# Performance work log

Measured on AMD Instinct MI355X. Metric: run time of the kernel, lower is better.

The kernel has to match this reference:

```python
import jax, jax.numpy as jnp
import numpy as np

B, L, R, A, E = 256, 64, 1024, 512, 1024


def lstm_cell(x, h, c, W_ih, W_hh, b_ih, b_hh):
    # PyTorch LSTMCell gate order: i, f, g, o
    gates = x @ W_ih.T + b_ih + h @ W_hh.T + b_hh
    i, f, g, o = jnp.split(gates, 4, axis=1)
    c2 = jax.nn.sigmoid(f) * c + jax.nn.sigmoid(i) * jnp.tanh(g)
    h2 = jax.nn.sigmoid(o) * jnp.tanh(c2)
    return h2, c2


def attend(h, wh_w, wh_b, wa_w, wa_b, feats_proj, feats_value):
    # Bahdanau attention: tanh(Wh h + proj(feats)) -> scalar logit -> softmax -> weighted sum
    dot = jnp.tanh(feats_proj + (h @ wh_w.T + wh_b)[:, None, :])  # [B,L,A]
    logits = jnp.einsum('bla,a->bl', dot, wa_w[0]) + wa_b[0]      # [B,L]
    w = jax.nn.softmax(logits, axis=1)
    return jnp.einsum('bl,bld->bd', w, feats_value)


def setup_inputs() -> dict:
    key = jax.random.key(0)
    ks = iter(jax.random.split(key, 64))
    rn = lambda shape, s=1.0: jax.random.normal(next(ks), shape, dtype=jnp.float32) * s
    inp = {
        'xt': rn((B, E)),
        'fc_feats': rn((B, R)),
        'roi_feats': rn((B, L, R)),
        'p_roi_feats': rn((B, L, A)),
        'context_feats': rn((B, L, R)),
        'state_h': rn((2, B, R)),
        'state_c': rn((2, B, R)),
        # scco (visual) LSTM: input E + 2R
        'W_ih_v': rn((4 * R, E + 2 * R), 0.02), 'W_hh_v': rn((4 * R, R), 0.02),
        'b_ih_v': rn((4 * R,), 0.02), 'b_hh_v': rn((4 * R,), 0.02),
        # language LSTM: input 2R
        'W_ih_l': rn((4 * R, 2 * R), 0.02), 'W_hh_l': rn((4 * R, R), 0.02),
        'b_ih_l': rn((4 * R,), 0.02), 'b_hh_l': rn((4 * R,), 0.02),
        # SingleSP: wh, wa
        'sp_wh_w': rn((A, R), 0.02), 'sp_wh_b': rn((A,), 0.02),
        'sp_wa_w': rn((1, A), 0.02), 'sp_wa_b': rn((1,), 0.02),
        # ContextSP: wh, wv, wa
        'ctx_wh_w': rn((A, R), 0.02), 'ctx_wh_b': rn((A,), 0.02),
        'ctx_wv_w': rn((A, R), 0.02), 'ctx_wv_b': rn((A,), 0.02),
        'ctx_wa_w': rn((1, A), 0.02), 'ctx_wa_b': rn((1,), 0.02),
        # CompSP: wh, wv, wa
        'cmp_wh_w': rn((A, R), 0.02), 'cmp_wh_b': rn((A,), 0.02),
        'cmp_wv_w': rn((A, R), 0.02), 'cmp_wv_b': rn((A,), 0.02),
        'cmp_wa_w': rn((1, A), 0.02), 'cmp_wa_b': rn((1,), 0.02),
        # OutputSP: wv, wh, wa
        'out_wv_w': rn((A, R), 0.02), 'out_wv_b': rn((A,), 0.02),
        'out_wh_w': rn((A, R), 0.02), 'out_wh_b': rn((A,), 0.02),
        'out_wa_w': rn((1, A), 0.02), 'out_wa_b': rn((1,), 0.02),
    }
    return inp


def reference(xt, fc_feats, roi_feats, p_roi_feats, context_feats, state_h, state_c,
              W_ih_v, W_hh_v, b_ih_v, b_hh_v, W_ih_l, W_hh_l, b_ih_l, b_hh_l,
              sp_wh_w, sp_wh_b, sp_wa_w, sp_wa_b,
              ctx_wh_w, ctx_wh_b, ctx_wv_w, ctx_wv_b, ctx_wa_w, ctx_wa_b,
              cmp_wh_w, cmp_wh_b, cmp_wv_w, cmp_wv_b, cmp_wa_w, cmp_wa_b,
              out_wv_w, out_wv_b, out_wh_w, out_wh_b, out_wa_w, out_wa_b):
    prev_h = state_h[-1]
    env = jnp.concatenate([prev_h, fc_feats, xt], axis=1)  # [B, 2R+E]
    h_vis, c_vis = lstm_cell(env, state_h[0], state_c[0], W_ih_v, W_hh_v, b_ih_v, b_hh_v)

    # SingleSP: attend over rois using precomputed projections p_roi_feats
    single_feat = attend(h_vis, sp_wh_w, sp_wh_b, sp_wa_w, sp_wa_b, p_roi_feats, roi_feats)

    # ContextSP: attend over context_feats
    ctx_proj = context_feats @ ctx_wv_w.T + ctx_wv_b
    context_feat = attend(h_vis, ctx_wh_w, ctx_wh_b, ctx_wa_w, ctx_wa_b, ctx_proj, context_feats)

    # CompSP: attend over relation feats = context - roi
    rel = context_feat[:, None, :] - roi_feats  # [B,L,R]
    rel_proj = rel @ cmp_wv_w.T + cmp_wv_b
    comp_feat = attend(h_vis, cmp_wh_w, cmp_wh_b, cmp_wa_w, cmp_wa_b, rel_proj, rel)

    # OutputSP: attend over {single, comp, fc}
    feats3 = jnp.stack([single_feat, comp_feat, fc_feats], axis=1)  # [B,3,R]
    f3_proj = feats3 @ out_wv_w.T + out_wv_b
    output_feats = attend(h_vis, out_wh_w, out_wh_b, out_wa_w, out_wa_b, f3_proj, feats3)

    lang_in = jnp.concatenate([output_feats, h_vis], axis=1)  # [B,2R]
    h_lang, c_lang = lstm_cell(lang_in, state_h[1], state_c[1], W_ih_l, W_hh_l, b_ih_l, b_hh_l)

    output = h_lang  # dropout is identity in eval mode
    new_h = jnp.stack([h_vis, h_lang])
    new_c = jnp.stack([c_vis, c_lang])
    return output, new_h, new_c, output_feats
```

## Files before the change

kernel.cpp:

```cpp
#include <hip/hip_runtime.h>
#include <hip/hip_bf16.h>
#include <math.h>

#define B_ 256
#define L_ 64
#define R_ 1024
#define A_ 512
#define E_ 1024
#define BR (B_ * R_)

typedef __attribute__((ext_vector_type(8))) short short8;
typedef __attribute__((ext_vector_type(4))) float f32x4;

__device__ __forceinline__ unsigned int pkbf(float x, float y) {
    union { __hip_bfloat162 h; unsigned int u; } cv;
    cv.h = __float22bfloat162_rn(make_float2(x, y));
    return cv.u;
}

__device__ __forceinline__ float tanh_fast(float x) {
    return 1.f - 2.f / (1.f + __expf(2.f * x));
}
__device__ __forceinline__ float sigm_(float x) { return 1.f / (1.f + __expf(-x)); }

__device__ __forceinline__ void mm_core(const float* __restrict__ Abm, int lda,
                                        const float* __restrict__ Wbn, int ldw,
                                        int K, f32x4 acc[4][4])
{
    __shared__ unsigned int As[2][2048];
    __shared__ unsigned int Ws[2][2048];

    const int t = threadIdx.x;
    const int srow = t >> 3, sub = t & 7;
    const int half = sub & 1;
    const int csw = (sub >> 1) ^ ((srow >> 1) & 3);
    int sidx[4];
    const float* pa[4];
    const float* pw[4];
#pragma unroll
    for (int i = 0; i < 4; ++i) {
        int row = srow + 32 * i;
        sidx[i] = row * 16 + csw * 4 + half * 2;
        pa[i] = Abm + (size_t)row * lda + sub * 4;
        pw[i] = Wbn + (size_t)row * ldw + sub * 4;
    }
    const int w = t >> 6, lane = t & 63;
    const int m0 = (w >> 1) * 64, n0 = (w & 1) * 64;
    const int lrow = lane & 15, quad = lane >> 4;
    int aidx[4], widx[4];
#pragma unroll
    for (int i = 0; i < 4; ++i) {
        int ra = m0 + i * 16 + lrow;
        aidx[i] = ra * 16 + ((quad ^ ((ra >> 1) & 3)) << 2);
        int rw = n0 + i * 16 + lrow;
        widx[i] = rw * 16 + ((quad ^ ((rw >> 1) & 3)) << 2);
    }

    float4 ra4[4], rw4[4];
#define MMC_LOAD() do { _Pragma("unroll") for (int i = 0; i < 4; ++i) { \
        ra4[i] = *(const float4*)pa[i]; rw4[i] = *(const float4*)pw[i]; \
        pa[i] += 32; pw[i] += 32; } } while (0)
#define MMC_STORE(buf) do { _Pragma("unroll") for (int i = 0; i < 4; ++i) { \
        *(uint2*)(As[buf] + sidx[i]) = make_uint2(pkbf(ra4[i].x, ra4[i].y), pkbf(ra4[i].z, ra4[i].w)); \
        *(uint2*)(Ws[buf] + sidx[i]) = make_uint2(pkbf(rw4[i].x, rw4[i].y), pkbf(rw4[i].z, rw4[i].w)); } } while (0)

    const int n = K >> 5;
    MMC_LOAD();
    MMC_STORE(0);
    MMC_LOAD();
    for (int k = 0; k < n; ++k) {
        __syncthreads();
        short8 af[4], wf[4];
#pragma unroll
        for (int i = 0; i < 4; ++i) {
            af[i] = *(const short8*)(As[k & 1] + aidx[i]);
            wf[i] = *(const short8*)(Ws[k & 1] + widx[i]);
        }
        if (k + 1 < n) {
            MMC_STORE((k + 1) & 1);
            if (k + 2 < n) MMC_LOAD();
        }
#pragma unroll
        for (int mt = 0; mt < 4; ++mt)
#pragma unroll
            for (int nt = 0; nt < 4; ++nt)
                acc[mt][nt] = __builtin_amdgcn_mfma_f32_16x16x32_bf16(
                    af[mt], wf[nt], acc[mt][nt], 0, 0, 0);
    }
#undef MMC_LOAD
#undef MMC_STORE
}

__device__ __forceinline__ void mm_store(f32x4 acc[4][4], float* __restrict__ Cbm,
                                         int ldc, int bn, const float* __restrict__ bias)
{
    const int t = threadIdx.x;
    const int w = t >> 6, lane = t & 63;
    const int m0 = (w >> 1) * 64, n0 = (w & 1) * 64;
    const int lrow = lane & 15, quad = lane >> 4;
#pragma unroll
    for (int nt = 0; nt < 4; ++nt) {
        int col = bn + n0 + nt * 16 + lrow;
        float bv = bias ? bias[col] : 0.f;
#pragma unroll
        for (int mt = 0; mt < 4; ++mt) {
            int rbase = m0 + mt * 16 + quad * 4;
#pragma unroll
            for (int r = 0; r < 4; ++r)
                Cbm[(size_t)(rbase + r) * ldc + col] = acc[mt][nt][r] + bv;
        }
    }
}

__device__ __forceinline__ void attn_epilogue(
    f32x4 acc[4][4], int bm, int bn, int M, int L,
    const float* __restrict__ base, const float* __restrict__ base2,
    const float* __restrict__ wbias, const float* __restrict__ wa,
    float sign, float* __restrict__ lpart)
{
    __shared__ float lsum[2][128];
    const int t = threadIdx.x;
    const int w = t >> 6, lane = t & 63;
    const int m0 = (w >> 1) * 64, n0 = (w & 1) * 64;
    const int lrow = lane & 15, quad = lane >> 4;
    float wav[4], wbv[4];
    int colv[4];
#pragma unroll
    for (int nt = 0; nt < 4; ++nt) {
        colv[nt] = bn + n0 + nt * 16 + lrow;
        wav[nt] = wa[colv[nt]];
        wbv[nt] = wbias ? wbias[colv[nt]] : 0.f;
    }
#pragma unroll
    for (int mt = 0; mt < 4; ++mt) {
#pragma unroll
        for (int r = 0; r < 4; ++r) {
            int rl = m0 + mt * 16 + quad * 4 + r;
            int row = bm + rl;
            int b = row / L;
            const float* bp = base + (size_t)b * A_;
            const float* bp2 = base2 ? base2 + (size_t)b * A_ : nullptr;
            float s = 0.f;
#pragma unroll
            for (int nt = 0; nt < 4; ++nt) {
                float v = bp[colv[nt]] + wbv[nt] + sign * acc[mt][nt][r];
                if (bp2) v += bp2[colv[nt]];
                s += tanh_fast(v) * wav[nt];
            }
            s += __shfl_xor(s, 1);
            s += __shfl_xor(s, 2);
            s += __shfl_xor(s, 4);
            s += __shfl_xor(s, 8);
            if (lrow == 0) lsum[w & 1][rl] = s;
        }
    }
    __syncthreads();
    if (t < 128)
        lpart[(size_t)(bn >> 7) * M + bm + t] = lsum[0][t] + lsum[1][t];
}

struct Seg8 { const float* A[8]; const float* W[8]; int lda[8]; int ldw[8]; };

__global__ __launch_bounds__(256) void mm_seg(Seg8 s, float* __restrict__ Cbase,
                                              int ldc, int kchunk, int zstride)
{
    int z = blockIdx.z;
    int bm = blockIdx.y * 128, bn = blockIdx.x * 128;
    f32x4 acc[4][4];
#pragma unroll
    for (int i = 0; i < 4; ++i)
#pragma unroll
        for (int j = 0; j < 4; ++j) acc[i][j] = (f32x4)0.f;
    mm_core(s.A[z] + (size_t)bm * s.lda[z], s.lda[z],
            s.W[z] + (size_t)bn * s.ldw[z], s.ldw[z], kchunk, acc);
    mm_store(acc, Cbase + (size_t)z * zstride + (size_t)bm * ldc, ldc, bn, nullptr);
}

struct Jobs4 { const float* A[4]; const float* W[4]; const float* bias[4]; float* C[4]; };
__global__ __launch_bounds__(256) void mm_jobs(Jobs4 p, int K)
{
    int z = blockIdx.z;
    int bm = blockIdx.y * 128, bn = blockIdx.x * 128;
    f32x4 acc[4][4];
#pragma unroll
    for (int i = 0; i < 4; ++i)
#pragma unroll
        for (int j = 0; j < 4; ++j) acc[i][j] = (f32x4)0.f;
    mm_core(p.A[z] + (size_t)bm * 1024, 1024, p.W[z] + (size_t)bn * 1024, 1024, K, acc);
    mm_store(acc, p.C[z] + (size_t)bm * 512, 512, bn, p.bias[z]);
}

__global__ __launch_bounds__(256) void mm_fused_attn(
    const float* __restrict__ A, int lda, const float* __restrict__ W, int ldw, int K,
    const float* __restrict__ base, const float* __restrict__ base2,
    const float* __restrict__ wbias, const float* __restrict__ wa,
    float sign, int M, int L, float* __restrict__ lpart)
{
    int bm = blockIdx.y * 128, bn = blockIdx.x * 128;
    f32x4 acc[4][4];
#pragma unroll
    for (int i = 0; i < 4; ++i)
#pragma unroll
        for (int j = 0; j < 4; ++j) acc[i][j] = (f32x4)0.f;
    mm_core(A + (size_t)bm * lda, lda, W + (size_t)bn * ldw, ldw, K, acc);
    attn_epilogue(acc, bm, bn, M, L, base, base2, wbias, wa, sign, lpart);
}

__global__ __launch_bounds__(256) void attn_logits_sp(
    const float* __restrict__ base, const float* __restrict__ proj,
    const float* __restrict__ wa, float* __restrict__ logits)
{
    int idx = blockIdx.x * 4 + (threadIdx.x >> 6);
    int lane = threadIdx.x & 63;
    int b = idx >> 6;
    const f32x4* p = (const f32x4*)(proj + (size_t)idx * A_);
    const f32x4* bs = (const f32x4*)(base + (size_t)b * A_);
    const f32x4* wv = (const f32x4*)wa;
    float acc = 0.f;
#pragma unroll
    for (int i = 0; i < 2; ++i) {
        int a = i * 64 + lane;
        f32x4 pv = p[a], bv = bs[a], w4 = wv[a];
#pragma unroll
        for (int j = 0; j < 4; ++j) acc += tanh_fast(bv[j] + pv[j]) * w4[j];
    }
#pragma unroll
    for (int off = 32; off > 0; off >>= 1) acc += __shfl_xor(acc, off);
    if (lane == 0) logits[idx] = acc;
}

__global__ __launch_bounds__(256) void softmax_part(
    const float* __restrict__ lpart, int np, int M, int L, float* __restrict__ attw)
{
    int grp = blockIdx.x * 4 + (threadIdx.x >> 6);
    int lane = threadIdx.x & 63;
    int row = grp * L + lane;
    float v = -INFINITY;
    if (lane < L) {
        float s = 0.f;
        for (int p = 0; p < np; ++p) s += lpart[(size_t)p * M + row];
        v = s;
    }
    float m = v;
#pragma unroll
    for (int off = 32; off > 0; off >>= 1) m = fmaxf(m, __shfl_xor(m, off));
    float e = (lane < L) ? __expf(v - m) : 0.f;
    float s = e;
#pragma unroll
    for (int off = 32; off > 0; off >>= 1) s += __shfl_xor(s, off);
    if (lane < L) attw[row] = e / s;
}

__global__ void ws_one(const float* __restrict__ wgt, const float* __restrict__ V,
                       float* __restrict__ out)
{
    int idx = blockIdx.x * blockDim.x + threadIdx.x;
    int b = idx >> 8, d4 = idx & 255;
    const f32x4* vp = (const f32x4*)(V + (size_t)b * L_ * R_) + d4;
    const float* wp = wgt + b * L_;
    f32x4 acc = (f32x4)0.f;
    for (int l = 0; l < L_; ++l) acc += wp[l] * vp[(size_t)l * 256];
    ((f32x4*)out)[idx] = acc;
}

__global__ void ws_dual(const float* __restrict__ w1, const float* __restrict__ w2,
                        const float* __restrict__ V, const float* __restrict__ ctx,
                        float* __restrict__ out1, float* __restrict__ out2)
{
    int idx = blockIdx.x * blockDim.x + threadIdx.x;
    int b = idx >> 8, d4 = idx & 255;
    const f32x4* vp = (const f32x4*)(V + (size_t)b * L_ * R_) + d4;
    const float* p1 = w1 + b * L_;
    const float* p2 = w2 + b * L_;
    f32x4 a1 = (f32x4)0.f, a2 = (f32x4)0.f;
    for (int l = 0; l < L_; ++l) {
        f32x4 v = vp[(size_t)l * 256];
        a1 += p1[l] * v;
        a2 += p2[l] * v;
    }
    ((f32x4*)out1)[idx] = a1;
    ((f32x4*)out2)[idx] = ((const f32x4*)ctx)[idx] - a2;
}

__global__ void ws_out_k(const float* __restrict__ wgt, const float* __restrict__ f3,
                         float* __restrict__ out)
{
    int idx = blockIdx.x * blockDim.x + threadIdx.x;
    int b = idx >> 8, d4 = idx & 255;
    const f32x4* fp = (const f32x4*)f3;
    f32x4 acc = (f32x4)0.f;
#pragma unroll
    for (int j = 0; j < 3; ++j)
        acc += wgt[b * 3 + j] * fp[(size_t)(b * 3 + j) * 256 + d4];
    ((f32x4*)out)[idx] = acc;
}

__global__ void build_feats3(const float* __restrict__ sf, const float* __restrict__ cf,
                             const float* __restrict__ fc, float* __restrict__ f3)
{
    int idx = blockIdx.x * blockDim.x + threadIdx.x;
    int d4 = idx & 255;
    int tt = idx >> 8;
    int j = tt % 3, b = tt / 3;
    const float* src = (j == 0) ? sf : (j == 1) ? cf : fc;
    ((f32x4*)f3)[idx] = ((const f32x4*)(src + (size_t)b * R_))[d4];
}

__global__ void lstm_pw(const float* __restrict__ gp, int P,
                        const float* __restrict__ b_ih, const float* __restrict__ b_hh,
                        const float* __restrict__ c_prev,
                        float* __restrict__ h_out, float* __restrict__ h_out2,
                        float* __restrict__ c_out)
{
    int idx = blockIdx.x * blockDim.x + threadIdx.x;
    int b = idx >> 8, r4 = idx & 255;
    f32x4 g[4];
#pragma unroll
    for (int gi = 0; gi < 4; ++gi) {
        int o = gi * 256 + r4;
        f32x4 s = ((const f32x4*)b_ih)[o] + ((const f32x4*)b_hh)[o];
        for (int p = 0; p < P; ++p)
            s += ((const f32x4*)(gp + (size_t)p * B_ * 4096 + (size_t)b * 4096))[o];
        g[gi] = s;
    }
    f32x4 cp = ((const f32x4*)c_prev)[idx];
    f32x4 c2, h2;
#pragma unroll
    for (int j = 0; j < 4; ++j) {
        float cc = sigm_(g[1][j]) * cp[j] + sigm_(g[0][j]) * tanh_fast(g[2][j]);
        c2[j] = cc;
        h2[j] = sigm_(g[3][j]) * tanh_fast(cc);
    }
    ((f32x4*)c_out)[idx] = c2;
    ((f32x4*)h_out)[idx] = h2;
    if (h_out2) ((f32x4*)h_out2)[idx] = h2;
}

extern "C" void kernel_launch(void* const* d_in, const int* in_sizes, int n_in,
                              void* d_out, int out_size, void* d_ws, size_t ws_size,
                              hipStream_t stream)
{
    const float* xt      = (const float*)d_in[0];
    const float* fc      = (const float*)d_in[1];
    const float* roi     = (const float*)d_in[2];
    const float* p_roi   = (const float*)d_in[3];
    const float* ctxf    = (const float*)d_in[4];
    const float* sh      = (const float*)d_in[5];
    const float* sc      = (const float*)d_in[6];
    const float* W_ih_v  = (const float*)d_in[7];
    const float* W_hh_v  = (const float*)d_in[8];
    const float* b_ih_v  = (const float*)d_in[9];
    const float* b_hh_v  = (const float*)d_in[10];
    const float* W_ih_l  = (const float*)d_in[11];
    const float* W_hh_l  = (const float*)d_in[12];
    const float* b_ih_l  = (const float*)d_in[13];
    const float* b_hh_l  = (const float*)d_in[14];
    const float* sp_wh_w = (const float*)d_in[15];
    const float* sp_wh_b = (const float*)d_in[16];
    const float* sp_wa_w = (const float*)d_in[17];
    const float* ctx_wh_w= (const float*)d_in[19];
    const float* ctx_wh_b= (const float*)d_in[20];
    const float* ctx_wv_w= (const float*)d_in[21];
    const float* ctx_wv_b= (const float*)d_in[22];
    const float* ctx_wa_w= (const float*)d_in[23];
    const float* cmp_wh_w= (const float*)d_in[25];
    const float* cmp_wh_b= (const float*)d_in[26];
    const float* cmp_wv_w= (const float*)d_in[27];
    const float* cmp_wv_b= (const float*)d_in[28];
    const float* cmp_wa_w= (const float*)d_in[29];
    const float* out_wv_w= (const float*)d_in[31];
    const float* out_wv_b= (const float*)d_in[32];
    const float* out_wh_w= (const float*)d_in[33];
    const float* out_wh_b= (const float*)d_in[34];
    const float* out_wa_w= (const float*)d_in[35];

    float* out = (float*)d_out;
    float* h_vis    = out + BR;
    float* h_lang   = out;
    float* h_lang2  = out + 2 * BR;
    float* c_vis    = out + 3 * BR;
    float* c_lang   = out + 4 * BR;
    float* out_feats= out + 5 * BR;

    float* ws = (float*)d_ws;
    float* gates      = ws;
    float* hproj4     = gates + (size_t)8 * B_ * 4096;
    float* base_cmp2  = hproj4 + (size_t)4 * B_ * A_;
    float* lpart      = base_cmp2 + (size_t)B_ * A_;
    float* lpart_out  = lpart + 4 * 16384;
    float* logits_sp  = lpart_out + 4 * 768;
    float* attw_sp    = logits_sp + 16384;
    float* attw_ctx   = attw_sp + 16384;
    float* attw_cmp   = attw_ctx + 16384;
    float* attw_out   = attw_cmp + 16384;
    float* single_feat= attw_out + 768;
    float* context_feat = single_feat + BR;
    float* comp_feat  = context_feat + BR;
    float* feats3     = comp_feat + BR;

    float* hp0 = hproj4;
    float* hp1 = hproj4 + (size_t)B_ * A_;
    float* hp2 = hproj4 + (size_t)2 * B_ * A_;
    float* hp3 = hproj4 + (size_t)3 * B_ * A_;

    const dim3 blk(256);
    const int ZST = B_ * 4096;

    {
        Seg8 s;
        s.A[0] = sh + BR;       s.W[0] = W_ih_v;          s.lda[0] = 1024; s.ldw[0] = 3072;
        s.A[1] = sh + BR + 512; s.W[1] = W_ih_v + 512;    s.lda[1] = 1024; s.ldw[1] = 3072;
        s.A[2] = fc;            s.W[2] = W_ih_v + 1024;   s.lda[2] = 1024; s.ldw[2] = 3072;
        s.A[3] = fc + 512;      s.W[3] = W_ih_v + 1536;   s.lda[3] = 1024; s.ldw[3] = 3072;
        s.A[4] = xt;            s.W[4] = W_ih_v + 2048;   s.lda[4] = 1024; s.ldw[4] = 3072;
        s.A[5] = xt + 512;      s.W[5] = W_ih_v + 2560;   s.lda[5] = 1024; s.ldw[5] = 3072;
        s.A[6] = sh;            s.W[6] = W_hh_v;          s.lda[6] = 1024; s.ldw[6] = 1024;
        s.A[7] = sh + 512;      s.W[7] = W_hh_v + 512;    s.lda[7] = 1024; s.ldw[7] = 1024;
        mm_seg<<<dim3(32, 2, 8), blk, 0, stream>>>(s, gates, 4096, 512, ZST);
    }
    lstm_pw<<<dim3(B_), blk, 0, stream>>>(gates, 8, b_ih_v, b_hh_v, sc, h_vis, nullptr, c_vis);

    {
        Jobs4 p;
        p.A[0] = h_vis; p.W[0] = sp_wh_w;  p.bias[0] = sp_wh_b;  p.C[0] = hp0;
        p.A[1] = h_vis; p.W[1] = ctx_wh_w; p.bias[1] = ctx_wh_b; p.C[1] = hp1;
        p.A[2] = h_vis; p.W[2] = cmp_wh_w; p.bias[2] = cmp_wh_b; p.C[2] = hp2;
        p.A[3] = h_vis; p.W[3] = out_wh_w; p.bias[3] = out_wh_b; p.C[3] = hp3;
        mm_jobs<<<dim3(4, 2, 4), blk, 0, stream>>>(p, 1024);
    }

    attn_logits_sp<<<dim3(B_ * L_ / 4), blk, 0, stream>>>(hp0, p_roi, sp_wa_w, logits_sp);
    softmax_part<<<dim3(64), blk, 0, stream>>>(logits_sp, 1, 16384, 64, attw_sp);

    mm_fused_attn<<<dim3(4, 128), blk, 0, stream>>>(ctxf, 1024, ctx_wv_w, 1024, 1024,
                                                    hp1, nullptr, ctx_wv_b, ctx_wa_w,
                                                    1.f, 16384, 64, lpart);
    softmax_part<<<dim3(64), blk, 0, stream>>>(lpart, 4, 16384, 64, attw_ctx);
    ws_one<<<dim3(B_), blk, 0, stream>>>(attw_ctx, ctxf, context_feat);

    {
        Jobs4 p;
        p.A[0] = p.A[1] = p.A[2] = p.A[3] = context_feat;
        p.W[0] = p.W[1] = p.W[2] = p.W[3] = cmp_wv_w;
        p.bias[0] = p.bias[1] = p.bias[2] = p.bias[3] = cmp_wv_b;
        p.C[0] = p.C[1] = p.C[2] = p.C[3] = base_cmp2;
        mm_jobs<<<dim3(4, 2, 1), blk, 0, stream>>>(p, 1024);
    }
    mm_fused_attn<<<dim3(4, 128), blk, 0, stream>>>(roi, 1024, cmp_wv_w, 1024, 1024,
                                                    hp2, base_cmp2, nullptr, cmp_wa_w,
                                                    -1.f, 16384, 64, lpart);
    softmax_part<<<dim3(64), blk, 0, stream>>>(lpart, 4, 16384, 64, attw_cmp);
    ws_dual<<<dim3(B_), blk, 0, stream>>>(attw_sp, attw_cmp, roi, context_feat,
                                          single_feat, comp_feat);

    build_feats3<<<dim3(B_ * 3), blk, 0, stream>>>(single_feat, comp_feat, fc, feats3);
    mm_fused_attn<<<dim3(4, 6), blk, 0, stream>>>(feats3, 1024, out_wv_w, 1024, 1024,
                                                  hp3, nullptr, out_wv_b, out_wa_w,
                                                  1.f, 768, 3, lpart_out);
    softmax_part<<<dim3(64), blk, 0, stream>>>(lpart_out, 4, 768, 3, attw_out);
    ws_out_k<<<dim3(B_), blk, 0, stream>>>(attw_out, feats3, out_feats);

    {
        Seg8 s;
        s.A[0] = out_feats;       s.W[0] = W_ih_l;        s.lda[0] = 1024; s.ldw[0] = 2048;
        s.A[1] = out_feats + 512; s.W[1] = W_ih_l + 512;  s.lda[1] = 1024; s.ldw[1] = 2048;
        s.A[2] = h_vis;           s.W[2] = W_ih_l + 1024; s.lda[2] = 1024; s.ldw[2] = 2048;
        s.A[3] = h_vis + 512;     s.W[3] = W_ih_l + 1536; s.lda[3] = 1024; s.ldw[3] = 2048;
        s.A[4] = sh + BR;         s.W[4] = W_hh_l;        s.lda[4] = 1024; s.ldw[4] = 1024;
        s.A[5] = sh + BR + 512;   s.W[5] = W_hh_l + 512;  s.lda[5] = 1024; s.ldw[5] = 1024;
        s.A[6] = s.A[5];          s.W[6] = s.W[5];        s.lda[6] = 1024; s.ldw[6] = 1024;
        s.A[7] = s.A[5];          s.W[7] = s.W[5];        s.lda[7] = 1024; s.ldw[7] = 1024;
        mm_seg<<<dim3(32, 2, 6), blk, 0, stream>>>(s, gates, 4096, 512, ZST);
    }
    lstm_pw<<<dim3(B_), blk, 0, stream>>>(gates, 6, b_ih_l, b_hh_l, sc + BR,
                                          h_lang, h_lang2, c_lang);
}
```

Measured before the change: 588.0 us.

## Stage GEMM tiles via direct global-to-LDS loads and swizzle block order

The shared GEMM core now copies fp32 tiles straight from global memory into LDS with global_load_lds, using an XOR-swizzled layout. It converts to bf16 when fragments are read from LDS instead of converting in registers before the LDS store. This removes register staging and the separate store step, at the cost of doubling LDS footprint (fp32 tiles) and doing conversions per fragment read. Block indices are also remapped across the grid in strides of eight, which changes which tiles run concurrently and may affect cache locality.

```diff
diff --git a/kernel.cpp b/kernel.cpp
--- a/kernel.cpp
+++ b/kernel.cpp
@@ -23,62 +23,82 @@
 }
 __device__ __forceinline__ float sigm_(float x) { return 1.f / (1.f + __expf(-x)); }
 
+__device__ __forceinline__ void gl16(const float* g, float* l) {
+    __builtin_amdgcn_global_load_lds(
+        (const __attribute__((address_space(1))) void*)g,
+        (__attribute__((address_space(3))) void*)l, 16, 0, 0);
+}
+
+__device__ __forceinline__ short8 pack8(f32x4 a, f32x4 b) {
+    union { unsigned int u[4]; short8 s; } r;
+    r.u[0] = pkbf(a[0], a[1]); r.u[1] = pkbf(a[2], a[3]);
+    r.u[2] = pkbf(b[0], b[1]); r.u[3] = pkbf(b[2], b[3]);
+    return r.s;
+}
+
+__device__ __forceinline__ void swz3(int& bx, int& by, int& bz) {
+    int gx = gridDim.x, gy = gridDim.y, gz = gridDim.z;
+    int id = (blockIdx.z * gy + blockIdx.y) * gx + blockIdx.x;
+    int nwg = gx * gy * gz;
+    id = (id & 7) * (nwg >> 3) + (id >> 3);
+    bx = id % gx; id /= gx;
+    by = id % gy; bz = id / gy;
+}
+
 __device__ __forceinline__ void mm_core(const float* __restrict__ Abm, int lda,
                                         const float* __restrict__ Wbn, int ldw,
                                         int K, f32x4 acc[4][4])
 {
-    __shared__ unsigned int As[2][2048];
-    __shared__ unsigned int Ws[2][2048];
+    __shared__ float As[2][4096];
+    __shared__ float Ws[2][4096];
 
     const int t = threadIdx.x;
-    const int srow = t >> 3, sub = t & 7;
-    const int half = sub & 1;
-    const int csw = (sub >> 1) ^ ((srow >> 1) & 3);
-    int sidx[4];
+    const int w = t >> 6, lane = t & 63;
+
+    const int lr = lane >> 3;
+    const int csw = (lane & 7) ^ lr;
     const float* pa[4];
     const float* pw[4];
-#pragma unroll
-    for (int i = 0; i < 4; ++i) {
-        int row = srow + 32 * i;
-        sidx[i] = row * 16 + csw * 4 + half * 2;
-        pa[i] = Abm + (size_t)row * lda + sub * 4;
-        pw[i] = Wbn + (size_t)row * ldw + sub * 4;
-    }
-    const int w = t >> 6, lane = t & 63;
+    int ldst[4];
+#pragma unroll
+    for (int r = 0; r < 4; ++r) {
+        int row = 32 * r + 8 * w + lr;
+        pa[r] = Abm + (size_t)row * lda + csw * 4;
+        pw[r] = Wbn + (size_t)row * ldw + csw * 4;
+        ldst[r] = w * 256 + r * 1024;
+    }
+#define MMC_STAGE(buf, kof) do { _Pragma("unroll") \
+    for (int r = 0; r < 4; ++r) { \
+        gl16(pa[r] + (kof), &As[buf][ldst[r]]); \
+        gl16(pw[r] + (kof), &Ws[buf][ldst[r]]); } } while (0)
+
     const int m0 = (w >> 1) * 64, n0 = (w & 1) * 64;
     const int lrow = lane & 15, quad = lane >> 4;
-    int aidx[4], widx[4];
+    int ai[4], wi[4];
 #pragma unroll
     for (int i = 0; i < 4; ++i) {
         int ra = m0 + i * 16 + lrow;
-        aidx[i] = ra * 16 + ((quad ^ ((ra >> 1) & 3)) << 2);
+        ai[i] = ra * 32 + ((((quad << 1) ^ (lrow & 7)) & 7) << 2);
         int rw = n0 + i * 16 + lrow;
-        widx[i] = rw * 16 + ((quad ^ ((rw >> 1) & 3)) << 2);
-    }
-
-    float4 ra4[4], rw4[4];
-#define MMC_LOAD() do { _Pragma("unroll") for (int i = 0; i < 4; ++i) { \
-        ra4[i] = *(const float4*)pa[i]; rw4[i] = *(const float4*)pw[i]; \
-        pa[i] += 32; pw[i] += 32; } } while (0)
-#define MMC_STORE(buf) do { _Pragma("unroll") for (int i = 0; i < 4; ++i) { \
-        *(uint2*)(As[buf] + sidx[i]) = make_uint2(pkbf(ra4[i].x, ra4[i].y), pkbf(ra4[i].z, ra4[i].w)); \
-        *(uint2*)(Ws[buf] + sidx[i]) = make_uint2(pkbf(rw4[i].x, rw4[i].y), pkbf(rw4[i].z, rw4[i].w)); } } while (0)
+        wi[i] = rw * 32 + ((((quad << 1) ^ (lrow & 7)) & 7) << 2);
+    }
 
     const int n = K >> 5;
-    MMC_LOAD();
-    MMC_STORE(0);
-    MMC_LOAD();
+    MMC_STAGE(0, 0);
     for (int k = 0; k < n; ++k) {
         __syncthreads();
+        if (k + 1 < n) MMC_STAGE((k + 1) & 1, (k + 1) * 32);
+        const float* Ab = As[k & 1];
+        const float* Wb = Ws[k & 1];
         short8 af[4], wf[4];
 #pragma unroll
         for (int i = 0; i < 4; ++i) {
-            af[i] = *(const short8*)(As[k & 1] + aidx[i]);
-            wf[i] = *(const short8*)(Ws[k & 1] + widx[i]);
-        }
-        if (k + 1 < n) {
-            MMC_STORE((k + 1) & 1);
-            if (k + 2 < n) MMC_LOAD();
+            f32x4 a0 = *(const f32x4*)(Ab + ai[i]);
+            f32x4 a1 = *(const f32x4*)(Ab + (ai[i] ^ 4));
+            af[i] = pack8(a0, a1);
+            f32x4 w0 = *(const f32x4*)(Wb + wi[i]);
+            f32x4 w1 = *(const f32x4*)(Wb + (wi[i] ^ 4));
+            wf[i] = pack8(w0, w1);
         }
 #pragma unroll
         for (int mt = 0; mt < 4; ++mt)
@@ -87,8 +107,7 @@
                 acc[mt][nt] = __builtin_amdgcn_mfma_f32_16x16x32_bf16(
                     af[mt], wf[nt], acc[mt][nt], 0, 0, 0);
     }
-#undef MMC_LOAD
-#undef MMC_STORE
+#undef MMC_STAGE
 }
 
 __device__ __forceinline__ void mm_store(f32x4 acc[4][4], float* __restrict__ Cbm,
@@ -164,8 +183,10 @@
 __global__ __launch_bounds__(256) void mm_seg(Seg8 s, float* __restrict__ Cbase,
                                               int ldc, int kchunk, int zstride)
 {
-    int z = blockIdx.z;
-    int bm = blockIdx.y * 128, bn = blockIdx.x * 128;
+    int bx, by, bz;
+    swz3(bx, by, bz);
+    int z = bz;
+    int bm = by * 128, bn = bx * 128;
     f32x4 acc[4][4];
 #pragma unroll
     for (int i = 0; i < 4; ++i)
@@ -179,8 +200,10 @@
 struct Jobs4 { const float* A[4]; const float* W[4]; const float* bias[4]; float* C[4]; };
 __global__ __launch_bounds__(256) void mm_jobs(Jobs4 p, int K)
 {
-    int z = blockIdx.z;
-    int bm = blockIdx.y * 128, bn = blockIdx.x * 128;
+    int bx, by, bz;
+    swz3(bx, by, bz);
+    int z = bz;
+    int bm = by * 128, bn = bx * 128;
     f32x4 acc[4][4];
 #pragma unroll
     for (int i = 0; i < 4; ++i)
@@ -196,7 +219,9 @@
     const float* __restrict__ wbias, const float* __restrict__ wa,
     float sign, int M, int L, float* __restrict__ lpart)
 {
-    int bm = blockIdx.y * 128, bn = blockIdx.x * 128;
+    int bx, by, bz;
+    swz3(bx, by, bz);
+    int bm = by * 128, bn = bx * 128;
     f32x4 acc[4][4];
 #pragma unroll
     for (int i = 0; i < 4; ++i)
```

Result: slower. 665.4 us (+13.2%).

## Halve GEMM M-tile to 64 rows and add XCD-aware block swizzle

Applied to the files above, without the earlier changes.

Shrinks the per-block M tile of the shared bf16 MFMA GEMM core from 128 to 64 rows, which halves the A shared-memory buffer and the accumulators, and doubles every GEMM launch grid along M. The goal is to fill the CUs better on the small launches (gate projections, hidden projections, output attention) and to raise occupancy. A block-id remap spreads consecutive tiles across the 8 XCDs so neighbouring tiles land on different XCDs. In exchange, each block reuses the weight tile over fewer rows, so more global and L2 traffic goes to weights.

```diff
diff --git a/kernel.cpp b/kernel.cpp
--- a/kernel.cpp
+++ b/kernel.cpp
@@ -23,46 +23,65 @@
 }
 __device__ __forceinline__ float sigm_(float x) { return 1.f / (1.f + __expf(-x)); }
 
+__device__ __forceinline__ void swz3(int& bx, int& by, int& bz) {
+    int gx = gridDim.x, gy = gridDim.y, gz = gridDim.z;
+    int id = (blockIdx.z * gy + blockIdx.y) * gx + blockIdx.x;
+    int nwg = gx * gy * gz;
+    id = (id & 7) * (nwg >> 3) + (id >> 3);
+    bx = id % gx; id /= gx;
+    by = id % gy; bz = id / gy;
+}
+
 __device__ __forceinline__ void mm_core(const float* __restrict__ Abm, int lda,
                                         const float* __restrict__ Wbn, int ldw,
-                                        int K, f32x4 acc[4][4])
-{
-    __shared__ unsigned int As[2][2048];
+                                        int K, f32x4 acc[2][4])
+{
+    __shared__ unsigned int As[2][1024];
     __shared__ unsigned int Ws[2][2048];
 
     const int t = threadIdx.x;
     const int srow = t >> 3, sub = t & 7;
     const int half = sub & 1;
     const int csw = (sub >> 1) ^ ((srow >> 1) & 3);
-    int sidx[4];
-    const float* pa[4];
+    int sidxA[2], sidxW[4];
+    const float* pa[2];
     const float* pw[4];
+#pragma unroll
+    for (int i = 0; i < 2; ++i) {
+        int row = srow + 32 * i;
+        sidxA[i] = row * 16 + csw * 4 + half * 2;
+        pa[i] = Abm + (size_t)row * lda + sub * 4;
+    }
 #pragma unroll
     for (int i = 0; i < 4; ++i) {
         int row = srow + 32 * i;
-        sidx[i] = row * 16 + csw * 4 + half * 2;
-        pa[i] = Abm + (size_t)row * lda + sub * 4;
+        sidxW[i] = row * 16 + csw * 4 + half * 2;
         pw[i] = Wbn + (size_t)row * ldw + sub * 4;
     }
     const int w = t >> 6, lane = t & 63;
-    const int m0 = (w >> 1) * 64, n0 = (w & 1) * 64;
+    const int m0 = (w >> 1) * 32, n0 = (w & 1) * 64;
     const int lrow = lane & 15, quad = lane >> 4;
-    int aidx[4], widx[4];
-#pragma unroll
-    for (int i = 0; i < 4; ++i) {
+    int aidx[2], widx[4];
+#pragma unroll
+    for (int i = 0; i < 2; ++i) {
         int ra = m0 + i * 16 + lrow;
         aidx[i] = ra * 16 + ((quad ^ ((ra >> 1) & 3)) << 2);
+    }
+#pragma unroll
+    for (int i = 0; i < 4; ++i) {
         int rw = n0 + i * 16 + lrow;
         widx[i] = rw * 16 + ((quad ^ ((rw >> 1) & 3)) << 2);
     }
 
-    float4 ra4[4], rw4[4];
-#define MMC_LOAD() do { _Pragma("unroll") for (int i = 0; i < 4; ++i) { \
-        ra4[i] = *(const float4*)pa[i]; rw4[i] = *(const float4*)pw[i]; \
-        pa[i] += 32; pw[i] += 32; } } while (0)
-#define MMC_STORE(buf) do { _Pragma("unroll") for (int i = 0; i < 4; ++i) { \
-        *(uint2*)(As[buf] + sidx[i]) = make_uint2(pkbf(ra4[i].x, ra4[i].y), pkbf(ra4[i].z, ra4[i].w)); \
-        *(uint2*)(Ws[buf] + sidx[i]) = make_uint2(pkbf(rw4[i].x, rw4[i].y), pkbf(rw4[i].z, rw4[i].w)); } } while (0)
+    float4 ra4[2], rw4[4];
+#define MMC_LOAD() do { _Pragma("unroll") for (int i = 0; i < 2; ++i) { \
+        ra4[i] = *(const float4*)pa[i]; pa[i] += 32; } \
+        _Pragma("unroll") for (int i = 0; i < 4; ++i) { \
+        rw4[i] = *(const float4*)pw[i]; pw[i] += 32; } } while (0)
+#define MMC_STORE(buf) do { _Pragma("unroll") for (int i = 0; i < 2; ++i) \
+        *(uint2*)(As[buf] + sidxA[i]) = make_uint2(pkbf(ra4[i].x, ra4[i].y), pkbf(ra4[i].z, ra4[i].w)); \
+        _Pragma("unroll") for (int i = 0; i < 4; ++i) \
+        *(uint2*)(Ws[buf] + sidxW[i]) = make_uint2(pkbf(rw4[i].x, rw4[i].y), pkbf(rw4[i].z, rw4[i].w)); } while (0)
 
     const int n = K >> 5;
     MMC_LOAD();
@@ -70,18 +89,17 @@
     MMC_LOAD();
     for (int k = 0; k < n; ++k) {
         __syncthreads();
-        short8 af[4], wf[4];
-#pragma unroll
-        for (int i = 0; i < 4; ++i) {
-            af[i] = *(const short8*)(As[k & 1] + aidx[i]);
-            wf[i] = *(const short8*)(Ws[k & 1] + widx[i]);
-        }
+        short8 af[2], wf[4];
+#pragma unroll
+        for (int i = 0; i < 2; ++i) af[i] = *(const short8*)(As[k & 1] + aidx[i]);
+#pragma unroll
+        for (int i = 0; i < 4; ++i) wf[i] = *(const short8*)(Ws[k & 1] + widx[i]);
         if (k + 1 < n) {
             MMC_STORE((k + 1) & 1);
             if (k + 2 < n) MMC_LOAD();
         }
 #pragma unroll
-        for (int mt = 0; mt < 4; ++mt)
+        for (int mt = 0; mt < 2; ++mt)
 #pragma unroll
             for (int nt = 0; nt < 4; ++nt)
                 acc[mt][nt] = __builtin_amdgcn_mfma_f32_16x16x32_bf16(
@@ -91,19 +109,19 @@
 #undef MMC_STORE
 }
 
-__device__ __forceinline__ void mm_store(f32x4 acc[4][4], float* __restrict__ Cbm,
+__device__ __forceinline__ void mm_store(f32x4 acc[2][4], float* __restrict__ Cbm,
                                          int ldc, int bn, const float* __restrict__ bias)
 {
     const int t = threadIdx.x;
     const int w = t >> 6, lane = t & 63;
-    const int m0 = (w >> 1) * 64, n0 = (w & 1) * 64;
+    const int m0 = (w >> 1) * 32, n0 = (w & 1) * 64;
     const int lrow = lane & 15, quad = lane >> 4;
 #pragma unroll
     for (int nt = 0; nt < 4; ++nt) {
         int col = bn + n0 + nt * 16 + lrow;
         float bv = bias ? bias[col] : 0.f;
 #pragma unroll
-        for (int mt = 0; mt < 4; ++mt) {
+        for (int mt = 0; mt < 2; ++mt) {
             int rbase = m0 + mt * 16 + quad * 4;
 #pragma unroll
             for (int r = 0; r < 4; ++r)
@@ -113,15 +131,15 @@
 }
 
 __device__ __forceinline__ void attn_epilogue(
-    f32x4 acc[4][4], int bm, int bn, int M, int L,
+    f32x4 acc[2][4], int bm, int bn, int M, int L,
     const float* __restrict__ base, const float* __restrict__ base2,
     const float* __restrict__ wbias, const float* __restrict__ wa,
     float sign, float* __restrict__ lpart)
 {
-    __shared__ float lsum[2][128];
+    __shared__ float lsum[2][64];
     const int t = threadIdx.x;
     const int w = t >> 6, lane = t & 63;
-    const int m0 = (w >> 1) * 64, n0 = (w & 1) * 64;
+    const int m0 = (w >> 1) * 32, n0 = (w & 1) * 64;
     const int lrow = lane & 15, quad = lane >> 4;
     float wav[4], wbv[4];
     int colv[4];
@@ -132,7 +150,7 @@
         wbv[nt] = wbias ? wbias[colv[nt]] : 0.f;
     }
 #pragma unroll
-    for (int mt = 0; mt < 4; ++mt) {
+    for (int mt = 0; mt < 2; ++mt) {
 #pragma unroll
         for (int r = 0; r < 4; ++r) {
             int rl = m0 + mt * 16 + quad * 4 + r;
@@ -155,7 +173,7 @@
         }
     }
     __syncthreads();
-    if (t < 128)
+    if (t < 64)
         lpart[(size_t)(bn >> 7) * M + bm + t] = lsum[0][t] + lsum[1][t];
 }
 
@@ -164,11 +182,13 @@
 __global__ __launch_bounds__(256) void mm_seg(Seg8 s, float* __restrict__ Cbase,
                                               int ldc, int kchunk, int zstride)
 {
-    int z = blockIdx.z;
-    int bm = blockIdx.y * 128, bn = blockIdx.x * 128;
-    f32x4 acc[4][4];
-#pragma unroll
-    for (int i = 0; i < 4; ++i)
+    int bx, by, bz;
+    swz3(bx, by, bz);
+    int z = bz;
+    int bm = by * 64, bn = bx * 128;
+    f32x4 acc[2][4];
+#pragma unroll
+    for (int i = 0; i < 2; ++i)
 #pragma unroll
         for (int j = 0; j < 4; ++j) acc[i][j] = (f32x4)0.f;
     mm_core(s.A[z] + (size_t)bm * s.lda[z], s.lda[z],
@@ -179,11 +199,13 @@
 struct Jobs4 { const float* A[4]; const float* W[4]; const float* bias[4]; float* C[4]; };
 __global__ __launch_bounds__(256) void mm_jobs(Jobs4 p, int K)
 {
-    int z = blockIdx.z;
-    int bm = blockIdx.y * 128, bn = blockIdx.x * 128;
-    f32x4 acc[4][4];
-#pragma unroll
-    for (int i = 0; i < 4; ++i)
+    int bx, by, bz;
+    swz3(bx, by, bz);
+    int z = bz;
+    int bm = by * 64, bn = bx * 128;
+    f32x4 acc[2][4];
+#pragma unroll
+    for (int i = 0; i < 2; ++i)
 #pragma unroll
         for (int j = 0; j < 4; ++j) acc[i][j] = (f32x4)0.f;
     mm_core(p.A[z] + (size_t)bm * 1024, 1024, p.W[z] + (size_t)bn * 1024, 1024, K, acc);
@@ -196,10 +218,12 @@
     const float* __restrict__ wbias, const float* __restrict__ wa,
     float sign, int M, int L, float* __restrict__ lpart)
 {
-    int bm = blockIdx.y * 128, bn = blockIdx.x * 128;
-    f32x4 acc[4][4];
-#pragma unroll
-    for (int i = 0; i < 4; ++i)
+    int bx, by, bz;
+    swz3(bx, by, bz);
+    int bm = by * 64, bn = bx * 128;
+    f32x4 acc[2][4];
+#pragma unroll
+    for (int i = 0; i < 2; ++i)
 #pragma unroll
         for (int j = 0; j < 4; ++j) acc[i][j] = (f32x4)0.f;
     mm_core(A + (size_t)bm * lda, lda, W + (size_t)bn * ldw, ldw, K, acc);
@@ -416,7 +440,7 @@
         s.A[5] = xt + 512;      s.W[5] = W_ih_v + 2560;   s.lda[5] = 1024; s.ldw[5] = 3072;
         s.A[6] = sh;            s.W[6] = W_hh_v;          s.lda[6] = 1024; s.ldw[6] = 1024;
         s.A[7] = sh + 512;      s.W[7] = W_hh_v + 512;    s.lda[7] = 1024; s.ldw[7] = 1024;
-        mm_seg<<<dim3(32, 2, 8), blk, 0, stream>>>(s, gates, 4096, 512, ZST);
+        mm_seg<<<dim3(32, 4, 8), blk, 0, stream>>>(s, gates, 4096, 512, ZST);
     }
     lstm_pw<<<dim3(B_), blk, 0, stream>>>(gates, 8, b_ih_v, b_hh_v, sc, h_vis, nullptr, c_vis);
 
@@ -426,13 +450,13 @@
         p.A[1] = h_vis; p.W[1] = ctx_wh_w; p.bias[1] = ctx_wh_b; p.C[1] = hp1;
         p.A[2] = h_vis; p.W[2] = cmp_wh_w; p.bias[2] = cmp_wh_b; p.C[2] = hp2;
         p.A[3] = h_vis; p.W[3] = out_wh_w; p.bias[3] = out_wh_b; p.C[3] = hp3;
-        mm_jobs<<<dim3(4, 2, 4), blk, 0, stream>>>(p, 1024);
+        mm_jobs<<<dim3(4, 4, 4), blk, 0, stream>>>(p, 1024);
     }
 
     attn_logits_sp<<<dim3(B_ * L_ / 4), blk, 0, stream>>>(hp0, p_roi, sp_wa_w, logits_sp);
     softmax_part<<<dim3(64), blk, 0, stream>>>(logits_sp, 1, 16384, 64, attw_sp);
 
-    mm_fused_attn<<<dim3(4, 128), blk, 0, stream>>>(ctxf, 1024, ctx_wv_w, 1024, 1024,
+    mm_fused_attn<<<dim3(4, 256), blk, 0, stream>>>(ctxf, 1024, ctx_wv_w, 1024, 1024,
                                                     hp1, nullptr, ctx_wv_b, ctx_wa_w,
                                                     1.f, 16384, 64, lpart);
     softmax_part<<<dim3(64), blk, 0, stream>>>(lpart, 4, 16384, 64, attw_ctx);
@@ -444,9 +468,9 @@
         p.W[0] = p.W[1] = p.W[2] = p.W[3] = cmp_wv_w;
         p.bias[0] = p.bias[1] = p.bias[2] = p.bias[3] = cmp_wv_b;
         p.C[0] = p.C[1] = p.C[2] = p.C[3] = base_cmp2;
-        mm_jobs<<<dim3(4, 2, 1), blk, 0, stream>>>(p, 1024);
-    }
-    mm_fused_attn<<<dim3(4, 128), blk, 0, stream>>>(roi, 1024, cmp_wv_w, 1024, 1024,
+        mm_jobs<<<dim3(4, 4, 1), blk, 0, stream>>>(p, 1024);
+    }
+    mm_fused_attn<<<dim3(4, 256), blk, 0, stream>>>(roi, 1024, cmp_wv_w, 1024, 1024,
                                                     hp2, base_cmp2, nullptr, cmp_wa_w,
                                                     -1.f, 16384, 64, lpart);
     softmax_part<<<dim3(64), blk, 0, stream>>>(lpart, 4, 16384, 64, attw_cmp);
@@ -454,9 +478,9 @@
                                           single_feat, comp_feat);
 
     build_feats3<<<dim3(B_ * 3), blk, 0, stream>>>(single_feat, comp_feat, fc, feats3);
-    mm_fused_attn<<<dim3(4, 6), blk, 0, stream>>>(feats3, 1024, out_wv_w, 1024, 1024,
-                                                  hp3, nullptr, out_wv_b, out_wa_w,
-                                                  1.f, 768, 3, lpart_out);
+    mm_fused_attn<<<dim3(4, 12), blk, 0, stream>>>(feats3, 1024, out_wv_w, 1024, 1024,
+                                                   hp3, nullptr, out_wv_b, out_wa_w,
+                                                   1.f, 768, 3, lpart_out);
     softmax_part<<<dim3(64), blk, 0, stream>>>(lpart_out, 4, 768, 3, attw_out);
     ws_out_k<<<dim3(B_), blk, 0, stream>>>(attw_out, feats3, out_feats);
 
@@ -470,7 +494,7 @@
         s.A[5] = sh + BR + 512;   s.W[5] = W_hh_l + 512;  s.lda[5] = 1024; s.ldw[5] = 1024;
         s.A[6] = s.A[5];          s.W[6] = s.W[5];        s.lda[6] = 1024; s.ldw[6] = 1024;
         s.A[7] = s.A[5];          s.W[7] = s.W[5];        s.lda[7] = 1024; s.ldw[7] = 1024;
-        mm_seg<<<dim3(32, 2, 6), blk, 0, stream>>>(s, gates, 4096, 512, ZST);
+        mm_seg<<<dim3(32, 4, 6), blk, 0, stream>>>(s, gates, 4096, 512, ZST);
     }
     lstm_pw<<<dim3(B_), blk, 0, stream>>>(gates, 6, b_ih_l, b_hh_l, sc + BR,
                                           h_lang, h_lang2, c_lang);
```

After: 598.1 us. About the same (+1.7%).
